# Kernel optimization log

Measured on AMD Instinct MI355X. Metric: run time of the kernel, lower is better.

Reference implementation:

```python
import jax, jax.numpy as jnp
import numpy as np

B, S, D, H = 4, 1024, 1024, 16
HD = D // H  # head_dim = 64


def _xavier(k, shape):
    fan_in, fan_out = shape[1], shape[0]
    limit = float(np.sqrt(6.0 / (fan_in + fan_out)))
    return jax.random.uniform(k, shape, jnp.float32, -limit, limit)


def setup_inputs() -> dict:
    key = jax.random.key(0)
    ks = jax.random.split(key, 12)
    inp = {
        "query": jax.random.normal(ks[0], (B, S, D), jnp.float32),
        "key": jax.random.normal(ks[1], (B, S, D), jnp.float32),
        "value": jax.random.normal(ks[2], (B, S, D), jnp.float32),
        "mask": jax.random.randint(ks[3], (B, 1, 1, S), 0, 2, jnp.int32),
        # Linear weights stored torch-style [out, in]; biases zero-ish (torch default uniform, use zeros-free small init)
        "Wq": _xavier(ks[4], (D, D)), "bq": jnp.zeros((D,), jnp.float32),
        "Wk": _xavier(ks[5], (D, D)), "bk": jnp.zeros((D,), jnp.float32),
        "Wv": _xavier(ks[6], (D, D)), "bv": jnp.zeros((D,), jnp.float32),
        "Wo": _xavier(ks[7], (D, D)), "bo": jnp.zeros((D,), jnp.float32),
    }
    return inp


def reference(query, key, value, mask, Wq, bq, Wk, bk, Wv, bv, Wo, bo):
    # Projections (torch Linear: x @ W.T + b)
    q = query @ Wq.T + bq
    k = key @ Wk.T + bk
    v = value @ Wv.T + bv
    # Split heads -> [B, H, S, HD]
    def split(x):
        b, s, _ = x.shape
        return x.reshape(b, s, H, HD).transpose(0, 2, 1, 3)
    q, k, v = split(q), split(k), split(v)
    scores = jnp.einsum('bhqd,bhkd->bhqk', q, k) / jnp.sqrt(jnp.float32(HD))
    scores = jnp.where(mask == 0, jnp.float32(-1e10), scores)
    attn = jax.nn.softmax(scores, axis=-1)  # dropout is identity in eval
    ctx = jnp.einsum('bhqk,bhkd->bhqd', attn, v)
    ctx = ctx.transpose(0, 2, 1, 3).reshape(ctx.shape[0], -1, D)
    out = ctx @ Wo.T + bo
    return out, attn
```

## Files before the change

### kernel.cpp

```cpp
#include <hip/hip_runtime.h>

constexpr int Bc = 4, Sc = 1024, Dc = 1024, Hc = 16, HDc = 64;
constexpr long BSD = (long)Bc * Sc * Dc;
constexpr long MM  = (long)Dc * Dc;

typedef __attribute__((ext_vector_type(8))) short bf16x8;
typedef __attribute__((ext_vector_type(4))) short bf16x4;
typedef __attribute__((ext_vector_type(4))) float f32x4;
typedef unsigned int u32;

__device__ inline ushort f2bf(float f) {
    union { float f; unsigned i; } v; v.f = f;
    unsigned lsb = (v.i >> 16) & 1;
    v.i += 0x7fffu + lsb;
    return (ushort)(v.i >> 16);
}

__global__ __launch_bounds__(256)
void cvt_all(const float* __restrict__ q, const float* __restrict__ k,
             const float* __restrict__ v, const float* __restrict__ Wq,
             const float* __restrict__ Wk, const float* __restrict__ Wv,
             const float* __restrict__ Wo, ushort* __restrict__ dst)
{
    const int t = blockIdx.y;
    const long n = (t < 3) ? BSD : MM;
    const long i = ((long)blockIdx.x * 256 + threadIdx.x) * 8;
    if (i >= n) return;
    const float* src; long off;
    switch (t) {
        case 0: src = q;  off = 0;            break;
        case 1: src = k;  off = BSD;          break;
        case 2: src = v;  off = 2 * BSD;      break;
        case 3: src = Wq; off = 3 * BSD;      break;
        case 4: src = Wk; off = 3 * BSD + MM; break;
        case 5: src = Wv; off = 3 * BSD + 2 * MM; break;
        default: src = Wo; off = 3 * BSD + 3 * MM; break;
    }
    f32x4 a = *(const f32x4*)(src + i);
    f32x4 b = *(const f32x4*)(src + i + 4);
    bf16x8 r;
    #pragma unroll
    for (int j = 0; j < 4; j++) { r[j] = (short)f2bf(a[j]); r[j + 4] = (short)f2bf(b[j]); }
    *(bf16x8*)(dst + off + i) = r;
}

__device__ inline void stage_tile(const ushort* __restrict__ G, int ld, int rowbase,
                                  int kt, ushort* lds, int wave, int lane)
{
    #pragma unroll
    for (int j = 0; j < 2; j++) {
        const int c = wave * 128 + j * 64 + lane;
        const int row = c >> 2, k8 = c & 3;
        const ushort* g = G + (long)(rowbase + row) * ld + kt + k8 * 8;
        ushort* l = lds + (wave * 128 + j * 64) * 8;
        __builtin_amdgcn_global_load_lds(
            (const __attribute__((address_space(1))) u32*)(const void*)g,
            (__attribute__((address_space(3))) u32*)(void*)l, 16, 0, 0);
    }
}

__device__ inline void gemm_core(const ushort* __restrict__ A, int lda,
                                 const ushort* __restrict__ Bt, int ldb, int K,
                                 int mtile, int ntile,
                                 ushort (*As)[128 * 32], ushort (*Bs)[128 * 32],
                                 f32x4 (*acc)[4], int wave, int lane)
{
    const int l15 = lane & 15, quad = lane >> 4;
    const int wr = wave >> 1, wc = wave & 1;

    stage_tile(A,  lda, mtile, 0, As[0], wave, lane);
    stage_tile(Bt, ldb, ntile, 0, Bs[0], wave, lane);
    __syncthreads();

    int buf = 0;
    for (int kt = 0; kt < K; kt += 32) {
        if (kt + 32 < K) {
            stage_tile(A,  lda, mtile, kt + 32, As[buf ^ 1], wave, lane);
            stage_tile(Bt, ldb, ntile, kt + 32, Bs[buf ^ 1], wave, lane);
        }
        bf16x8 af[4], bfr[4];
        #pragma unroll
        for (int mt = 0; mt < 4; mt++)
            af[mt] = *(const bf16x8*)(As[buf] + (wr * 64 + mt * 16 + l15) * 32 + quad * 8);
        #pragma unroll
        for (int nt = 0; nt < 4; nt++)
            bfr[nt] = *(const bf16x8*)(Bs[buf] + (wc * 64 + nt * 16 + l15) * 32 + quad * 8);
        #pragma unroll
        for (int mt = 0; mt < 4; mt++)
            #pragma unroll
            for (int nt = 0; nt < 4; nt++)
                acc[mt][nt] = __builtin_amdgcn_mfma_f32_16x16x32_bf16(af[mt], bfr[nt], acc[mt][nt], 0, 0, 0);
        __syncthreads();
        buf ^= 1;
    }
}

__global__ __launch_bounds__(256)
void gemm_qkv(const ushort* __restrict__ ws, const float* __restrict__ bq,
              const float* __restrict__ bk, const float* __restrict__ bv,
              ushort* __restrict__ QK, ushort* __restrict__ Vt)
{
    __shared__ ushort As[2][128 * 32];
    __shared__ ushort Bs[2][128 * 32];

    const int z = blockIdx.z;
    const ushort* A  = ws + (long)z * BSD;
    const ushort* Bt = ws + 3 * BSD + (long)z * MM;
    const float* bias = (z == 0) ? bq : (z == 1) ? bk : bv;

    const int lane = threadIdx.x & 63, wave = threadIdx.x >> 6;
    const int l15 = lane & 15, quad = lane >> 4;
    const int wr = wave >> 1, wc = wave & 1;
    const int mtile = blockIdx.y * 128, ntile = blockIdx.x * 128;

    f32x4 acc[4][4] = {};
    gemm_core(A, Dc, Bt, Dc, Dc, mtile, ntile, As, Bs, acc, wave, lane);

    #pragma unroll
    for (int mt = 0; mt < 4; mt++) {
        #pragma unroll
        for (int nt = 0; nt < 4; nt++) {
            const int col = ntile + wc * 64 + nt * 16 + l15;
            const float bb = bias[col];
            #pragma unroll
            for (int i = 0; i < 4; i++) {
                const int r = mtile + wr * 64 + mt * 16 + quad * 4 + i;
                const float vv = acc[mt][nt][i] + bb;
                if (z < 2) {
                    QK[(long)z * BSD + (long)r * Dc + col] = f2bf(vv);
                } else {
                    const int b = r >> 10, sI = r & 1023;
                    const int hh = col >> 6, dd = col & 63;
                    Vt[(long)((b * Hc + hh) * HDc + dd) * Sc + sI] = f2bf(vv);
                }
            }
        }
    }
}

__global__ __launch_bounds__(256)
void gemm_out(const ushort* __restrict__ A, const ushort* __restrict__ Bt,
              const float* __restrict__ bias, float* __restrict__ C)
{
    __shared__ ushort As[2][128 * 32];
    __shared__ ushort Bs[2][128 * 32];

    const int lane = threadIdx.x & 63, wave = threadIdx.x >> 6;
    const int l15 = lane & 15, quad = lane >> 4;
    const int wr = wave >> 1, wc = wave & 1;
    const int mtile = blockIdx.y * 128, ntile = blockIdx.x * 128;

    f32x4 acc[4][4] = {};
    gemm_core(A, Dc, Bt, Dc, Dc, mtile, ntile, As, Bs, acc, wave, lane);

    #pragma unroll
    for (int mt = 0; mt < 4; mt++) {
        #pragma unroll
        for (int nt = 0; nt < 4; nt++) {
            const int col = ntile + wc * 64 + nt * 16 + l15;
            const float bb = bias[col];
            #pragma unroll
            for (int i = 0; i < 4; i++) {
                const int r = mtile + wr * 64 + mt * 16 + quad * 4 + i;
                C[(long)r * Dc + col] = acc[mt][nt][i] + bb;
            }
        }
    }
}

__device__ inline int sc_idx(int row, int col) {
    return row * 1024 + ((((col >> 2) ^ (row & 7)) << 2) | (col & 3));
}

__global__ __launch_bounds__(256)
void attn_fused(const ushort* __restrict__ Q, const ushort* __restrict__ Kp,
                const ushort* __restrict__ Vt, const int* __restrict__ mask,
                float* __restrict__ attn, ushort* __restrict__ Ctx)
{
    __shared__ union { float f[16 * 1024]; ushort u[16 * 2048]; } sc;

    const int bh = blockIdx.y;
    const int b = bh >> 4, h = bh & 15;
    const int qbase = blockIdx.x * 16;
    const int lane = threadIdx.x & 63;
    const int wave = threadIdx.x >> 6;
    const int l15 = lane & 15, quad = lane >> 4;

    const ushort* Qh = Q  + (long)b * Sc * Dc + h * HDc;
    const ushort* Kh = Kp + (long)b * Sc * Dc + h * HDc;

    const ushort* qrow = Qh + (long)(qbase + l15) * Dc + quad * 8;
    const bf16x8 a0 = *(const bf16x8*)(qrow);
    const bf16x8 a1 = *(const bf16x8*)(qrow + 32);

    unsigned mbits = 0;
    {
        const int4* mp = (const int4*)(mask + b * Sc);
        #pragma unroll
        for (int jj = 0; jj < 4; jj++) {
            const int4 mm = mp[jj * 64 + lane];
            if (mm.x == 0) mbits |= 1u << (jj * 4 + 0);
            if (mm.y == 0) mbits |= 1u << (jj * 4 + 1);
            if (mm.z == 0) mbits |= 1u << (jj * 4 + 2);
            if (mm.w == 0) mbits |= 1u << (jj * 4 + 3);
        }
    }

    #pragma unroll 4
    for (int t = 0; t < 16; t++) {
        const int ct = wave * 16 + t;
        const ushort* krow = Kh + (long)(ct * 16 + l15) * Dc + quad * 8;
        const bf16x8 b0 = *(const bf16x8*)(krow);
        const bf16x8 b1 = *(const bf16x8*)(krow + 32);
        f32x4 acc = {};
        __builtin_amdgcn_s_setprio(1);
        acc = __builtin_amdgcn_mfma_f32_16x16x32_bf16(a0, b0, acc, 0, 0, 0);
        acc = __builtin_amdgcn_mfma_f32_16x16x32_bf16(a1, b1, acc, 0, 0, 0);
        __builtin_amdgcn_s_setprio(0);
        const int col = ct * 16 + l15;
        #pragma unroll
        for (int i = 0; i < 4; i++) sc.f[sc_idx(quad * 4 + i, col)] = acc[i];
    }
    __syncthreads();

    #pragma unroll 1
    for (int rr = 0; rr < 4; rr++) {
        const int r = wave * 4 + rr;
        const int sw = r & 7;
        float v[16];
        float mx = -3.0e38f;
        #pragma unroll
        for (int jj = 0; jj < 4; jj++) {
            const int c = jj * 64 + lane;
            const f32x4 x = *(const f32x4*)(sc.f + r * 1024 + ((c ^ sw) << 2));
            #pragma unroll
            for (int e = 0; e < 4; e++) {
                float s = x[e] * 0.125f;
                if (mbits & (1u << (jj * 4 + e))) s = -1e10f;
                v[jj * 4 + e] = s;
                mx = fmaxf(mx, s);
            }
        }
        #pragma unroll
        for (int off = 32; off >= 1; off >>= 1) mx = fmaxf(mx, __shfl_xor(mx, off, 64));
        float sum = 0.0f;
        #pragma unroll
        for (int i = 0; i < 16; i++) { v[i] = __expf(v[i] - mx); sum += v[i]; }
        #pragma unroll
        for (int off = 32; off >= 1; off >>= 1) sum += __shfl_xor(sum, off, 64);
        const float inv = 1.0f / sum;
        #pragma unroll
        for (int i = 0; i < 16; i++) v[i] *= inv;

        float* arow = attn + ((long)bh * Sc + qbase + r) * Sc + lane * 4;
        #pragma unroll
        for (int jj = 0; jj < 4; jj++) {
            f32x4 o;
            #pragma unroll
            for (int e = 0; e < 4; e++) o[e] = v[jj * 4 + e];
            *(f32x4*)(arow + jj * 256) = o;
        }

        ushort* prow = sc.u + r * 2048;
        const int sw2 = sw << 1;
        #pragma unroll
        for (int jj = 0; jj < 4; jj++) {
            const int u8 = jj * 64 + lane;
            bf16x4 pk;
            #pragma unroll
            for (int e = 0; e < 4; e++) pk[e] = (short)f2bf(v[jj * 4 + e]);
            *(bf16x4*)(prow + ((u8 ^ sw2) << 2)) = pk;
        }
    }
    __syncthreads();

    f32x4 pacc[4] = {};
    const ushort* prow = sc.u + l15 * 2048;
    const int sw2 = (l15 & 7) << 1;
    const ushort* Vh = Vt + (long)bh * HDc * Sc + (long)(wave * 16 + l15) * Sc + quad * 8;
    for (int k0 = 0; k0 < Sc; k0 += 128) {
        bf16x8 af[4], bv4[4];
        #pragma unroll
        for (int u = 0; u < 4; u++) {
            const int k = k0 + u * 32 + quad * 8;
            af[u]  = *(const bf16x8*)(prow + (((k >> 2) ^ sw2) << 2));
            bv4[u] = *(const bf16x8*)(Vh + k0 + u * 32);
        }
        __builtin_amdgcn_s_setprio(1);
        #pragma unroll
        for (int u = 0; u < 4; u++)
            pacc[u] = __builtin_amdgcn_mfma_f32_16x16x32_bf16(af[u], bv4[u], pacc[u], 0, 0, 0);
        __builtin_amdgcn_s_setprio(0);
    }
    f32x4 acc;
    #pragma unroll
    for (int i = 0; i < 4; i++) acc[i] = (pacc[0][i] + pacc[1][i]) + (pacc[2][i] + pacc[3][i]);

    const int dcol = h * HDc + wave * 16 + l15;
    #pragma unroll
    for (int i = 0; i < 4; i++) {
        const int r = qbase + quad * 4 + i;
        Ctx[(long)b * Sc * Dc + (long)r * Dc + dcol] = f2bf(acc[i]);
    }
}

extern "C" void kernel_launch(void* const* d_in, const int* in_sizes, int n_in,
                              void* d_out, int out_size, void* d_ws, size_t ws_size,
                              hipStream_t stream)
{
    const float* q    = (const float*)d_in[0];
    const float* k    = (const float*)d_in[1];
    const float* v    = (const float*)d_in[2];
    const int*   mask = (const int*)  d_in[3];
    const float* Wq   = (const float*)d_in[4];
    const float* bq   = (const float*)d_in[5];
    const float* Wk   = (const float*)d_in[6];
    const float* bk   = (const float*)d_in[7];
    const float* Wv   = (const float*)d_in[8];
    const float* bv   = (const float*)d_in[9];
    const float* Wo   = (const float*)d_in[10];
    const float* bo   = (const float*)d_in[11];

    ushort* ws  = (ushort*)d_ws;
    ushort* Wob = ws + 3 * BSD + 3 * MM;
    ushort* Qp  = ws + 3 * BSD + 4 * MM;
    ushort* Kpp = Qp + BSD;
    ushort* Vt  = Kpp + BSD;
    ushort* Ctx = Vt + BSD;

    float* out  = (float*)d_out;
    float* attn = out + BSD;

    const dim3 blk(256);

    cvt_all<<<dim3(BSD / (256 * 8), 7), blk, 0, stream>>>(q, k, v, Wq, Wk, Wv, Wo, ws);

    gemm_qkv<<<dim3(8, 32, 3), blk, 0, stream>>>(ws, bq, bk, bv, Qp, Vt);

    attn_fused<<<dim3(Sc / 16, Bc * Hc), blk, 0, stream>>>(Qp, Kpp, Vt, mask, attn, Ctx);

    gemm_out<<<dim3(8, 32), blk, 0, stream>>>(Ctx, Wob, bo, out);
}
```

Before: 537.6 us.

## Keep attention scores in registers and reduce softmax across waves via LDS

The QK^T scores now stay in registers (16 MFMA tiles per wave) rather than being staged as fp32 in a 64KB shared buffer. Softmax max and sum are computed per row with lane shuffles and a small cross-wave LDS reduction, and shared memory shrinks to a 32KB bf16 P buffer. With launch bounds set to 3 blocks per CU, the aim is higher occupancy and less LDS traffic. In exchange, the fp32 attn stores become scalar writes strided by row (16 lanes per row) instead of 16-byte vector stores, which can hurt global write coalescing.

```diff
diff --git a/kernel.cpp b/kernel.cpp
--- a/kernel.cpp
+++ b/kernel.cpp
@@ -5,7 +5,6 @@
 constexpr long MM  = (long)Dc * Dc;
 
 typedef __attribute__((ext_vector_type(8))) short bf16x8;
-typedef __attribute__((ext_vector_type(4))) short bf16x4;
 typedef __attribute__((ext_vector_type(4))) float f32x4;
 typedef unsigned int u32;
 
@@ -168,16 +167,13 @@
     }
 }
 
-__device__ inline int sc_idx(int row, int col) {
-    return row * 1024 + ((((col >> 2) ^ (row & 7)) << 2) | (col & 3));
-}
-
-__global__ __launch_bounds__(256)
+__global__ __launch_bounds__(256, 3)
 void attn_fused(const ushort* __restrict__ Q, const ushort* __restrict__ Kp,
                 const ushort* __restrict__ Vt, const int* __restrict__ mask,
                 float* __restrict__ attn, ushort* __restrict__ Ctx)
 {
-    __shared__ union { float f[16 * 1024]; ushort u[16 * 2048]; } sc;
+    __shared__ ushort pB[16 * 1024];
+    __shared__ float red[2][4][16];
 
     const int bh = blockIdx.y;
     const int b = bh >> 4, h = bh & 15;
@@ -193,19 +189,7 @@
     const bf16x8 a0 = *(const bf16x8*)(qrow);
     const bf16x8 a1 = *(const bf16x8*)(qrow + 32);
 
-    unsigned mbits = 0;
-    {
-        const int4* mp = (const int4*)(mask + b * Sc);
-        #pragma unroll
-        for (int jj = 0; jj < 4; jj++) {
-            const int4 mm = mp[jj * 64 + lane];
-            if (mm.x == 0) mbits |= 1u << (jj * 4 + 0);
-            if (mm.y == 0) mbits |= 1u << (jj * 4 + 1);
-            if (mm.z == 0) mbits |= 1u << (jj * 4 + 2);
-            if (mm.w == 0) mbits |= 1u << (jj * 4 + 3);
-        }
-    }
-
+    f32x4 sacc[16];
     #pragma unroll 4
     for (int t = 0; t < 16; t++) {
         const int ct = wave * 16 + t;
@@ -213,69 +197,85 @@
         const bf16x8 b0 = *(const bf16x8*)(krow);
         const bf16x8 b1 = *(const bf16x8*)(krow + 32);
         f32x4 acc = {};
-        __builtin_amdgcn_s_setprio(1);
         acc = __builtin_amdgcn_mfma_f32_16x16x32_bf16(a0, b0, acc, 0, 0, 0);
         acc = __builtin_amdgcn_mfma_f32_16x16x32_bf16(a1, b1, acc, 0, 0, 0);
-        __builtin_amdgcn_s_setprio(0);
-        const int col = ct * 16 + l15;
-        #pragma unroll
-        for (int i = 0; i < 4; i++) sc.f[sc_idx(quad * 4 + i, col)] = acc[i];
-    }
+        sacc[t] = acc;
+    }
+
+    unsigned mbits = 0;
+    #pragma unroll
+    for (int t = 0; t < 16; t++)
+        if (mask[b * Sc + (wave * 16 + t) * 16 + l15] == 0) mbits |= (1u << t);
+
+    float mx[4] = { -3.0e38f, -3.0e38f, -3.0e38f, -3.0e38f };
+    #pragma unroll
+    for (int t = 0; t < 16; t++) {
+        const bool msk = (mbits >> t) & 1;
+        #pragma unroll
+        for (int i = 0; i < 4; i++) {
+            float s = sacc[t][i] * 0.125f;
+            s = msk ? -1e10f : s;
+            sacc[t][i] = s;
+            mx[i] = fmaxf(mx[i], s);
+        }
+    }
+    #pragma unroll
+    for (int off = 1; off <= 8; off <<= 1)
+        #pragma unroll
+        for (int i = 0; i < 4; i++) mx[i] = fmaxf(mx[i], __shfl_xor(mx[i], off, 64));
+    if (l15 == 0)
+        #pragma unroll
+        for (int i = 0; i < 4; i++) red[0][wave][quad * 4 + i] = mx[i];
     __syncthreads();
-
-    #pragma unroll 1
-    for (int rr = 0; rr < 4; rr++) {
-        const int r = wave * 4 + rr;
-        const int sw = r & 7;
-        float v[16];
-        float mx = -3.0e38f;
-        #pragma unroll
-        for (int jj = 0; jj < 4; jj++) {
-            const int c = jj * 64 + lane;
-            const f32x4 x = *(const f32x4*)(sc.f + r * 1024 + ((c ^ sw) << 2));
-            #pragma unroll
-            for (int e = 0; e < 4; e++) {
-                float s = x[e] * 0.125f;
-                if (mbits & (1u << (jj * 4 + e))) s = -1e10f;
-                v[jj * 4 + e] = s;
-                mx = fmaxf(mx, s);
-            }
-        }
-        #pragma unroll
-        for (int off = 32; off >= 1; off >>= 1) mx = fmaxf(mx, __shfl_xor(mx, off, 64));
-        float sum = 0.0f;
-        #pragma unroll
-        for (int i = 0; i < 16; i++) { v[i] = __expf(v[i] - mx); sum += v[i]; }
-        #pragma unroll
-        for (int off = 32; off >= 1; off >>= 1) sum += __shfl_xor(sum, off, 64);
-        const float inv = 1.0f / sum;
-        #pragma unroll
-        for (int i = 0; i < 16; i++) v[i] *= inv;
-
-        float* arow = attn + ((long)bh * Sc + qbase + r) * Sc + lane * 4;
-        #pragma unroll
-        for (int jj = 0; jj < 4; jj++) {
-            f32x4 o;
-            #pragma unroll
-            for (int e = 0; e < 4; e++) o[e] = v[jj * 4 + e];
-            *(f32x4*)(arow + jj * 256) = o;
-        }
-
-        ushort* prow = sc.u + r * 2048;
-        const int sw2 = sw << 1;
-        #pragma unroll
-        for (int jj = 0; jj < 4; jj++) {
-            const int u8 = jj * 64 + lane;
-            bf16x4 pk;
-            #pragma unroll
-            for (int e = 0; e < 4; e++) pk[e] = (short)f2bf(v[jj * 4 + e]);
-            *(bf16x4*)(prow + ((u8 ^ sw2) << 2)) = pk;
-        }
-    }
+    #pragma unroll
+    for (int i = 0; i < 4; i++) {
+        float g = red[0][0][quad * 4 + i];
+        #pragma unroll
+        for (int w = 1; w < 4; w++) g = fmaxf(g, red[0][w][quad * 4 + i]);
+        mx[i] = g;
+    }
+
+    float sm[4] = { 0.f, 0.f, 0.f, 0.f };
+    #pragma unroll
+    for (int t = 0; t < 16; t++)
+        #pragma unroll
+        for (int i = 0; i < 4; i++) {
+            const float e = __expf(sacc[t][i] - mx[i]);
+            sacc[t][i] = e;
+            sm[i] += e;
+        }
+    #pragma unroll
+    for (int off = 1; off <= 8; off <<= 1)
+        #pragma unroll
+        for (int i = 0; i < 4; i++) sm[i] += __shfl_xor(sm[i], off, 64);
+    if (l15 == 0)
+        #pragma unroll
+        for (int i = 0; i < 4; i++) red[1][wave][quad * 4 + i] = sm[i];
     __syncthreads();
+    float inv[4];
+    #pragma unroll
+    for (int i = 0; i < 4; i++) {
+        float g = red[1][0][quad * 4 + i] + red[1][1][quad * 4 + i]
+                + red[1][2][quad * 4 + i] + red[1][3][quad * 4 + i];
+        inv[i] = 1.0f / g;
+    }
+
+    #pragma unroll
+    for (int t = 0; t < 16; t++) {
+        const int col = (wave * 16 + t) * 16 + l15;
+        #pragma unroll
+        for (int i = 0; i < 4; i++) {
+            const float p = sacc[t][i] * inv[i];
+            const int r = quad * 4 + i;
+            attn[((long)bh * Sc + qbase + r) * Sc + col] = p;
+            const int u = (col >> 2) ^ ((r & 7) << 1);
+            pB[r * 1024 + (u << 2) + (col & 3)] = f2bf(p);
+        }
+    }
+    __syncthreads();
 
     f32x4 pacc[4] = {};
-    const ushort* prow = sc.u + l15 * 2048;
+    const ushort* prow = pB + l15 * 1024;
     const int sw2 = (l15 & 7) << 1;
     const ushort* Vh = Vt + (long)bh * HDc * Sc + (long)(wave * 16 + l15) * Sc + quad * 8;
     for (int k0 = 0; k0 < Sc; k0 += 128) {
```

After: 694.0 us. +29.1%, slower.
